# Kernel tuning notes

Hardware: AMD Instinct MI355X
Metric: run time of the kernel (lower is better)

The kernel has to match this reference:

```python
import jax, jax.numpy as jnp
import numpy as np

B, T, D = 4, 2048, 1024
N_HEADS = 16
D_HEAD = D // N_HEADS


def setup_inputs() -> dict:
    key = jax.random.key(0)
    ks = jax.random.split(key, 5)
    s = 1.0 / np.sqrt(D)
    return {
        "x": jax.random.normal(ks[0], (B, T, D), dtype=jnp.float32),
        "wq": jax.random.normal(ks[1], (D, D), dtype=jnp.float32) * s,
        "wk": jax.random.normal(ks[2], (D, D), dtype=jnp.float32) * s,
        "wv": jax.random.normal(ks[3], (D, D), dtype=jnp.float32) * s,
        "wo": jax.random.normal(ks[4], (D, D), dtype=jnp.float32) * s,
    }


def reference(x, wq, wk, wv, wo):
    # nn.Linear applies y = x @ W^T (no bias)
    b, t, c = x.shape
    def heads(w):
        return (x @ w.T).reshape(b, t, N_HEADS, D_HEAD).transpose(0, 2, 1, 3)  # (B,H,T,d)
    q, k, v = heads(wq), heads(wk), heads(wv)
    scale = 1.0 / np.sqrt(D_HEAD).astype(np.float32)
    att = jnp.einsum('bhqd,bhkd->bhqk', q, k) * scale
    causal = jnp.tril(jnp.ones((t, t), dtype=bool))
    att = jnp.where(causal[None, None], att, -jnp.inf)
    att = jax.nn.softmax(att, axis=-1)
    # dropout is identity in eval / p acts as 0 for the deterministic reference
    y = jnp.einsum('bhqk,bhkd->bhqd', att, v)
    y = y.transpose(0, 2, 1, 3).reshape(b, t, c)
    return y @ wo.T
```

## Files before the change

### kernel.cpp

```cpp
#include <hip/hip_runtime.h>

#define B_ 4
#define T_ 2048
#define D_ 1024
#define H_ 16
#define DH_ 64
#define M_ (B_*T_)
#define KP 72

typedef __attribute__((ext_vector_type(8))) short short8;
typedef __attribute__((ext_vector_type(4))) float f32x4;
typedef __attribute__((ext_vector_type(4))) unsigned short u16x4;
typedef _Float16 half4f __attribute__((ext_vector_type(4)));

__device__ __forceinline__ unsigned short f2bf(float f) {
  unsigned int u = __float_as_uint(f);
  u += 0x7FFFu + ((u >> 16) & 1u);
  return (unsigned short)(u >> 16);
}

__device__ __forceinline__ void async_copy16(const void* g, void* l) {
  __builtin_amdgcn_global_load_lds(
      (const __attribute__((address_space(1))) unsigned int*)(g),
      (__attribute__((address_space(3))) unsigned int*)(l),
      16, 0, 0);
}

__device__ __forceinline__ f32x4 mfma32(short8 a, short8 b, f32x4 c) {
  return __builtin_amdgcn_mfma_f32_16x16x32_bf16(a, b, c, 0, 0, 0);
}

__global__ __launch_bounds__(256) void cvt_f32_to_bf16(
    const float* __restrict__ in, unsigned short* __restrict__ out, int n4) {
  int i = blockIdx.x * 256 + threadIdx.x;
  if (i >= n4) return;
  const float4 v = reinterpret_cast<const float4*>(in)[i];
  u16x4 o;
  o.x = f2bf(v.x); o.y = f2bf(v.y); o.z = f2bf(v.z); o.w = f2bf(v.w);
  reinterpret_cast<u16x4*>(out)[i] = o;
}

__global__ __launch_bounds__(256) void gemm_qkv(
    const unsigned short* __restrict__ A,
    const unsigned short* __restrict__ Wq,
    const unsigned short* __restrict__ Wk,
    const unsigned short* __restrict__ Wv,
    unsigned short* __restrict__ Qo,
    unsigned short* __restrict__ Ko,
    _Float16* __restrict__ Vo) {
  __shared__ __align__(16) unsigned short ldsA[128*32];
  __shared__ __align__(16) unsigned short ldsB[128*32];
  const int tid = threadIdx.x;
  const int w = tid >> 6, lane = tid & 63;
  const int quad = lane >> 4, l16 = lane & 15;
  const int wr = (w >> 1) * 64, wc = (w & 1) * 64;
  const int m0 = blockIdx.x * 128;
  const int seg = blockIdx.y >> 3;
  const int n0 = (blockIdx.y & 7) * 128;
  const unsigned short* Bt = (seg == 0) ? Wq : ((seg == 1) ? Wk : Wv);

  const unsigned short* gA = A  + (size_t)(m0 + w*32 + (lane >> 2)) * D_ + (lane & 3) * 8;
  const unsigned short* gB = Bt + (size_t)(n0 + w*32 + (lane >> 2)) * D_ + (lane & 3) * 8;
  unsigned short* lA = ldsA + (w*32)*32;
  unsigned short* lB = ldsB + (w*32)*32;

  f32x4 acc[4][4] = {};

  for (int k0 = 0; k0 < D_; k0 += 32) {
    __syncthreads();
#pragma unroll
    for (int g = 0; g < 2; ++g) {
      async_copy16(gA + (size_t)k0 + (size_t)g*16*D_, lA + g*16*32);
      async_copy16(gB + (size_t)k0 + (size_t)g*16*D_, lB + g*16*32);
    }
    __syncthreads();
    short8 af[4], bfr[4];
#pragma unroll
    for (int t = 0; t < 4; ++t) {
      af[t]  = *reinterpret_cast<const short8*>(ldsA + (wr + t*16 + l16)*32 + quad*8);
      bfr[t] = *reinterpret_cast<const short8*>(ldsB + (wc + t*16 + l16)*32 + quad*8);
    }
#pragma unroll
    for (int i = 0; i < 4; ++i)
#pragma unroll
      for (int j = 0; j < 4; ++j)
        acc[i][j] = mfma32(af[i], bfr[j], acc[i][j]);
  }

#pragma unroll
  for (int i = 0; i < 4; ++i) {
#pragma unroll
    for (int j = 0; j < 4; ++j) {
      if (seg == 2) {
        const int colc = n0 + wc + j*16 + l16;
        const int hh = colc >> 6, dd = colc & (DH_ - 1);
        const int row0 = m0 + wr + i*16 + quad*4;
        const int bb = row0 >> 11, t0 = row0 & (T_ - 1);
        half4f vh = {(_Float16)acc[i][j][0], (_Float16)acc[i][j][1],
                     (_Float16)acc[i][j][2], (_Float16)acc[i][j][3]};
        *reinterpret_cast<half4f*>(
            &Vo[(size_t)((bb*H_ + hh)*DH_ + dd)*T_ + t0]) = vh;
      } else {
        unsigned short* out = (seg == 0) ? Qo : Ko;
        const float scl = (seg == 0) ? (0.125f * 1.44269504089f) : 1.f;
#pragma unroll
        for (int r = 0; r < 4; ++r) {
          const int row = m0 + wr + i*16 + quad*4 + r;
          const int col = n0 + wc + j*16 + l16;
          out[(size_t)row * D_ + col] = f2bf(acc[i][j][r] * scl);
        }
      }
    }
  }
}

__global__ __launch_bounds__(256) void gemm_out(
    const unsigned short* __restrict__ A,
    const unsigned short* __restrict__ Bt,
    float* __restrict__ Cout) {
  __shared__ __align__(16) unsigned short ldsA[128*32];
  __shared__ __align__(16) unsigned short ldsB[128*32];
  const int tid = threadIdx.x;
  const int w = tid >> 6, lane = tid & 63;
  const int quad = lane >> 4, l16 = lane & 15;
  const int wr = (w >> 1) * 64, wc = (w & 1) * 64;
  const int m0 = blockIdx.x * 128, n0 = blockIdx.y * 128;

  const unsigned short* gA = A  + (size_t)(m0 + w*32 + (lane >> 2)) * D_ + (lane & 3) * 8;
  const unsigned short* gB = Bt + (size_t)(n0 + w*32 + (lane >> 2)) * D_ + (lane & 3) * 8;
  unsigned short* lA = ldsA + (w*32)*32;
  unsigned short* lB = ldsB + (w*32)*32;

  f32x4 acc[4][4] = {};
  for (int k0 = 0; k0 < D_; k0 += 32) {
    __syncthreads();
#pragma unroll
    for (int g = 0; g < 2; ++g) {
      async_copy16(gA + (size_t)k0 + (size_t)g*16*D_, lA + g*16*32);
      async_copy16(gB + (size_t)k0 + (size_t)g*16*D_, lB + g*16*32);
    }
    __syncthreads();
    short8 af[4], bfr[4];
#pragma unroll
    for (int t = 0; t < 4; ++t) {
      af[t]  = *reinterpret_cast<const short8*>(ldsA + (wr + t*16 + l16)*32 + quad*8);
      bfr[t] = *reinterpret_cast<const short8*>(ldsB + (wc + t*16 + l16)*32 + quad*8);
    }
#pragma unroll
    for (int i = 0; i < 4; ++i)
#pragma unroll
      for (int j = 0; j < 4; ++j)
        acc[i][j] = mfma32(af[i], bfr[j], acc[i][j]);
  }
#pragma unroll
  for (int i = 0; i < 4; ++i)
#pragma unroll
    for (int j = 0; j < 4; ++j)
#pragma unroll
      for (int r = 0; r < 4; ++r)
        Cout[(size_t)(m0 + wr + i*16 + quad*4 + r) * D_ + n0 + wc + j*16 + l16] =
            acc[i][j][r];
}

__global__ __launch_bounds__(256) void flash_attn(
    const unsigned short* __restrict__ Q,
    const unsigned short* __restrict__ K,
    const _Float16* __restrict__ Vt,
    unsigned short* __restrict__ Y) {
  __shared__ __align__(16) unsigned short Kl[2][64*KP];
  __shared__ __align__(16) _Float16      Vl[2][64*KP];
  const int px = blockIdx.x, h = blockIdx.y, b = blockIdx.z;
  const int tid = threadIdx.x;
  const int w = tid >> 6, lane = tid & 63, quad = lane >> 4, l16 = lane & 15;
  const int hc = h * DH_;
  const size_t bh = (size_t)(b*H_ + h);

  const int sr = tid >> 2, sc = tid & 3;
  const unsigned short* Kg0 = K + ((size_t)(b*T_) + sr) * D_ + hc + sc*16;
  const _Float16*       Vg0 = Vt + (bh*DH_ + sr) * T_ + sc*16;

  uint4 kr0, kr1, vr0, vr1;
  auto loadKV = [&](int kt) {
    const unsigned short* kg = Kg0 + (size_t)kt * 64 * D_;
    const _Float16*       vg = Vg0 + kt * 64;
    kr0 = *reinterpret_cast<const uint4*>(kg);
    kr1 = *reinterpret_cast<const uint4*>(kg + 8);
    vr0 = *reinterpret_cast<const uint4*>(vg);
    vr1 = *reinterpret_cast<const uint4*>(vg + 8);
  };
  auto writeKV = [&](int bi) {
    *reinterpret_cast<uint4*>(&Kl[bi][sr*KP + sc*16])     = kr0;
    *reinterpret_cast<uint4*>(&Kl[bi][sr*KP + sc*16 + 8]) = kr1;
    *reinterpret_cast<uint4*>(&Vl[bi][sr*KP + sc*16])     = vr0;
    *reinterpret_cast<uint4*>(&Vl[bi][sr*KP + sc*16 + 8]) = vr1;
  };

#pragma unroll
  for (int pi = 0; pi < 2; ++pi) {
    const int it = pi ? (31 - px) : px;
    const int qg0 = it*64 + w*16;

    short8 bq[2];
#pragma unroll
    for (int ks = 0; ks < 2; ++ks)
      bq[ks] = *reinterpret_cast<const short8*>(
          Q + (size_t)(b*T_ + qg0 + l16) * D_ + hc + ks*32 + quad*8);

    f32x4 o[4] = {};
    float rs = 0.f;
    const int ktmax = it;

    __syncthreads();
    loadKV(0);
    writeKV(0);
    __syncthreads();

    for (int kt = 0; kt <= ktmax; ++kt) {
      const int cur = kt & 1;
      if (kt < ktmax) loadKV(kt + 1);
      const bool diag = (kt == ktmax);
      const int smax = diag ? w : 3;
      const int diagS = diag ? w : -1;
      for (int s = 0; s <= smax; ++s) {
        const short8 ka0 = *reinterpret_cast<const short8*>(
            &Kl[cur][(s*16 + l16)*KP + quad*8]);
        const short8 ka1 = *reinterpret_cast<const short8*>(
            &Kl[cur][(s*16 + l16)*KP + 32 + quad*8]);
        f32x4 z = {0.f, 0.f, 0.f, 0.f};
        z = mfma32(ka0, bq[0], z);
        z = mfma32(ka1, bq[1], z);
        float p[4];
        const bool dsub = (s == diagS);
#pragma unroll
        for (int r = 0; r < 4; ++r) {
          float pv = __builtin_amdgcn_exp2f(z[r]);
          if (dsub && (quad*4 + r > l16)) pv = 0.f;
          p[r] = pv;
          rs += pv;
        }
        const half4f pf = {(_Float16)p[0], (_Float16)p[1],
                           (_Float16)p[2], (_Float16)p[3]};
#pragma unroll
        for (int dt = 0; dt < 4; ++dt) {
          const half4f vf = *reinterpret_cast<const half4f*>(
              &Vl[cur][(dt*16 + l16)*KP + s*16 + quad*4]);
          o[dt] = __builtin_amdgcn_mfma_f32_16x16x16f16(vf, pf, o[dt], 0, 0, 0);
        }
      }
      if (kt < ktmax) {
        __syncthreads();
        writeKV(cur ^ 1);
        __syncthreads();
      }
    }

    float rt = rs;
    rt += __shfl_xor(rt, 16);
    rt += __shfl_xor(rt, 32);
    const float inv = 1.f / rt;

#pragma unroll
    for (int dt = 0; dt < 4; ++dt) {
      u16x4 yo;
      yo.x = f2bf(o[dt][0] * inv);
      yo.y = f2bf(o[dt][1] * inv);
      yo.z = f2bf(o[dt][2] * inv);
      yo.w = f2bf(o[dt][3] * inv);
      *reinterpret_cast<u16x4*>(
          &Y[(size_t)(b*T_ + qg0 + l16) * D_ + hc + dt*16 + quad*4]) = yo;
    }
  }
}

extern "C" void kernel_launch(void* const* d_in, const int* in_sizes, int n_in,
                              void* d_out, int out_size, void* d_ws, size_t ws_size,
                              hipStream_t stream) {
  const float* x  = (const float*)d_in[0];
  const float* wq = (const float*)d_in[1];
  const float* wk = (const float*)d_in[2];
  const float* wv = (const float*)d_in[3];
  const float* wo = (const float*)d_in[4];

  unsigned short* xb  = (unsigned short*)d_ws;
  unsigned short* wqb = xb  + (size_t)M_ * D_;
  unsigned short* wkb = wqb + (size_t)D_ * D_;
  unsigned short* wvb = wkb + (size_t)D_ * D_;
  unsigned short* wob = wvb + (size_t)D_ * D_;
  unsigned short* q   = wob + (size_t)D_ * D_;
  unsigned short* k   = q   + (size_t)M_ * D_;
  _Float16*       vt  = (_Float16*)(k + (size_t)M_ * D_);
  unsigned short* y   = (unsigned short*)(vt + (size_t)M_ * D_);

  const int nx4 = M_ * D_ / 4, nw4 = D_ * D_ / 4;
  cvt_f32_to_bf16<<<nx4 / 256, 256, 0, stream>>>(x,  xb,  nx4);
  cvt_f32_to_bf16<<<nw4 / 256, 256, 0, stream>>>(wq, wqb, nw4);
  cvt_f32_to_bf16<<<nw4 / 256, 256, 0, stream>>>(wk, wkb, nw4);
  cvt_f32_to_bf16<<<nw4 / 256, 256, 0, stream>>>(wv, wvb, nw4);
  cvt_f32_to_bf16<<<nw4 / 256, 256, 0, stream>>>(wo, wob, nw4);

  gemm_qkv<<<dim3(M_ / 128, 24), 256, 0, stream>>>(xb, wqb, wkb, wvb, q, k, vt);

  flash_attn<<<dim3(16, H_, B_), 256, 0, stream>>>(q, k, vt, y);

  gemm_out<<<dim3(M_ / 128, D_ / 128), 256, 0, stream>>>(y, wob, (float*)d_out);
}
```

Baseline: 277.4 us.

## Give each attention wave two query tiles and fuse the five conversion kernels

The flash attention block drops to two waves of 128 threads, and each wave now handles 32 query rows as two 16-row tiles. Every K/V fragment read from LDS is therefore reused for twice as many MFMAs. The softmax row sum is now computed by an MFMA against a ones vector instead of scalar adds and shuffles, and the grid order changes so batch-head varies fastest. The five fp32-to-bf16 conversion launches are merged into one kernel to cut launch overhead. Trade-offs are higher register pressure, fewer waves per block to hide latency, and some wasted diagonal work.

```diff
diff --git a/kernel.cpp b/kernel.cpp
--- a/kernel.cpp
+++ b/kernel.cpp
@@ -29,15 +29,29 @@
 __device__ __forceinline__ f32x4 mfma32(short8 a, short8 b, f32x4 c) {
   return __builtin_amdgcn_mfma_f32_16x16x32_bf16(a, b, c, 0, 0, 0);
 }
-
-__global__ __launch_bounds__(256) void cvt_f32_to_bf16(
-    const float* __restrict__ in, unsigned short* __restrict__ out, int n4) {
+__device__ __forceinline__ f32x4 mfma16h(half4f a, half4f b, f32x4 c) {
+  return __builtin_amdgcn_mfma_f32_16x16x16f16(a, b, c, 0, 0, 0);
+}
+
+#define NX4 (M_*D_/4)
+#define NW4 (D_*D_/4)
+__global__ __launch_bounds__(256) void cvt_all(
+    const float* __restrict__ x,  const float* __restrict__ wq,
+    const float* __restrict__ wk, const float* __restrict__ wv,
+    const float* __restrict__ wo, unsigned short* __restrict__ xb,
+    unsigned short* __restrict__ wqb, unsigned short* __restrict__ wkb,
+    unsigned short* __restrict__ wvb, unsigned short* __restrict__ wob) {
   int i = blockIdx.x * 256 + threadIdx.x;
-  if (i >= n4) return;
-  const float4 v = reinterpret_cast<const float4*>(in)[i];
+  const float* src; unsigned short* dst; int off;
+  if (i < NX4)             { src = x;  dst = xb;  off = i; }
+  else if (i < NX4 + NW4)  { src = wq; dst = wqb; off = i - NX4; }
+  else if (i < NX4 + 2*NW4){ src = wk; dst = wkb; off = i - NX4 - NW4; }
+  else if (i < NX4 + 3*NW4){ src = wv; dst = wvb; off = i - NX4 - 2*NW4; }
+  else                     { src = wo; dst = wob; off = i - NX4 - 3*NW4; }
+  const float4 v = reinterpret_cast<const float4*>(src)[off];
   u16x4 o;
   o.x = f2bf(v.x); o.y = f2bf(v.y); o.z = f2bf(v.z); o.w = f2bf(v.w);
-  reinterpret_cast<u16x4*>(out)[i] = o;
+  reinterpret_cast<u16x4*>(dst)[off] = o;
 }
 
 __global__ __launch_bounds__(256) void gemm_qkv(
@@ -162,52 +176,58 @@
             acc[i][j][r];
 }
 
-__global__ __launch_bounds__(256) void flash_attn(
+__global__ __launch_bounds__(128) void flash_attn(
     const unsigned short* __restrict__ Q,
     const unsigned short* __restrict__ K,
     const _Float16* __restrict__ Vt,
     unsigned short* __restrict__ Y) {
   __shared__ __align__(16) unsigned short Kl[2][64*KP];
   __shared__ __align__(16) _Float16      Vl[2][64*KP];
-  const int px = blockIdx.x, h = blockIdx.y, b = blockIdx.z;
+  const int bh = blockIdx.x, px = blockIdx.y;
+  const int h = bh & (H_ - 1), b = bh >> 4;
   const int tid = threadIdx.x;
   const int w = tid >> 6, lane = tid & 63, quad = lane >> 4, l16 = lane & 15;
   const int hc = h * DH_;
-  const size_t bh = (size_t)(b*H_ + h);
-
-  const int sr = tid >> 2, sc = tid & 3;
-  const unsigned short* Kg0 = K + ((size_t)(b*T_) + sr) * D_ + hc + sc*16;
-  const _Float16*       Vg0 = Vt + (bh*DH_ + sr) * T_ + sc*16;
-
-  uint4 kr0, kr1, vr0, vr1;
+
+  const int sr = tid >> 1, sco = (tid & 1) * 32;
+  const unsigned short* Kg0 = K + ((size_t)(b*T_) + sr) * D_ + hc + sco;
+  const _Float16*       Vg0 = Vt + ((size_t)bh * DH_ + sr) * T_ + sco;
+
+  uint4 kr[4], vr[4];
   auto loadKV = [&](int kt) {
     const unsigned short* kg = Kg0 + (size_t)kt * 64 * D_;
     const _Float16*       vg = Vg0 + kt * 64;
-    kr0 = *reinterpret_cast<const uint4*>(kg);
-    kr1 = *reinterpret_cast<const uint4*>(kg + 8);
-    vr0 = *reinterpret_cast<const uint4*>(vg);
-    vr1 = *reinterpret_cast<const uint4*>(vg + 8);
+#pragma unroll
+    for (int j = 0; j < 4; ++j) {
+      kr[j] = *reinterpret_cast<const uint4*>(kg + j*8);
+      vr[j] = *reinterpret_cast<const uint4*>(vg + j*8);
+    }
   };
   auto writeKV = [&](int bi) {
-    *reinterpret_cast<uint4*>(&Kl[bi][sr*KP + sc*16])     = kr0;
-    *reinterpret_cast<uint4*>(&Kl[bi][sr*KP + sc*16 + 8]) = kr1;
-    *reinterpret_cast<uint4*>(&Vl[bi][sr*KP + sc*16])     = vr0;
-    *reinterpret_cast<uint4*>(&Vl[bi][sr*KP + sc*16 + 8]) = vr1;
+#pragma unroll
+    for (int j = 0; j < 4; ++j) {
+      *reinterpret_cast<uint4*>(&Kl[bi][sr*KP + sco + j*8]) = kr[j];
+      *reinterpret_cast<uint4*>(&Vl[bi][sr*KP + sco + j*8]) = vr[j];
+    }
   };
+
+  const half4f vones = {(_Float16)1.f, (_Float16)1.f, (_Float16)1.f, (_Float16)1.f};
 
 #pragma unroll
   for (int pi = 0; pi < 2; ++pi) {
     const int it = pi ? (31 - px) : px;
-    const int qg0 = it*64 + w*16;
-
-    short8 bq[2];
-#pragma unroll
-    for (int ks = 0; ks < 2; ++ks)
-      bq[ks] = *reinterpret_cast<const short8*>(
-          Q + (size_t)(b*T_ + qg0 + l16) * D_ + hc + ks*32 + quad*8);
-
-    f32x4 o[4] = {};
-    float rs = 0.f;
+    const int qg0 = it*64 + w*32;
+
+    short8 bq[2][2];
+#pragma unroll
+    for (int qt = 0; qt < 2; ++qt)
+#pragma unroll
+      for (int ks = 0; ks < 2; ++ks)
+        bq[qt][ks] = *reinterpret_cast<const short8*>(
+            Q + (size_t)(b*T_ + qg0 + qt*16 + l16) * D_ + hc + ks*32 + quad*8);
+
+    f32x4 o[2][4] = {};
+    f32x4 osum[2] = {};
     const int ktmax = it;
 
     __syncthreads();
@@ -219,32 +239,40 @@
       const int cur = kt & 1;
       if (kt < ktmax) loadKV(kt + 1);
       const bool diag = (kt == ktmax);
-      const int smax = diag ? w : 3;
-      const int diagS = diag ? w : -1;
+      const int smax = diag ? (2*w + 1) : 3;
       for (int s = 0; s <= smax; ++s) {
         const short8 ka0 = *reinterpret_cast<const short8*>(
             &Kl[cur][(s*16 + l16)*KP + quad*8]);
         const short8 ka1 = *reinterpret_cast<const short8*>(
             &Kl[cur][(s*16 + l16)*KP + 32 + quad*8]);
-        f32x4 z = {0.f, 0.f, 0.f, 0.f};
-        z = mfma32(ka0, bq[0], z);
-        z = mfma32(ka1, bq[1], z);
-        float p[4];
-        const bool dsub = (s == diagS);
-#pragma unroll
-        for (int r = 0; r < 4; ++r) {
-          float pv = __builtin_amdgcn_exp2f(z[r]);
-          if (dsub && (quad*4 + r > l16)) pv = 0.f;
-          p[r] = pv;
-          rs += pv;
+        const bool skip0 = diag && (s == 2*w + 1);
+        const bool m0d   = diag && (s == 2*w);
+        const bool m1d   = diag && (s == 2*w + 1);
+        half4f pf[2];
+#pragma unroll
+        for (int qt = 0; qt < 2; ++qt) {
+          if (qt == 0 && skip0) continue;
+          f32x4 z = {0.f, 0.f, 0.f, 0.f};
+          z = mfma32(ka0, bq[qt][0], z);
+          z = mfma32(ka1, bq[qt][1], z);
+          const bool dm = qt ? m1d : m0d;
+          float p[4];
+#pragma unroll
+          for (int r = 0; r < 4; ++r) {
+            float pv = __builtin_amdgcn_exp2f(z[r]);
+            if (dm && (quad*4 + r > l16)) pv = 0.f;
+            p[r] = pv;
+          }
+          pf[qt] = half4f{(_Float16)p[0], (_Float16)p[1],
+                          (_Float16)p[2], (_Float16)p[3]};
+          osum[qt] = mfma16h(vones, pf[qt], osum[qt]);
         }
-        const half4f pf = {(_Float16)p[0], (_Float16)p[1],
-                           (_Float16)p[2], (_Float16)p[3]};
 #pragma unroll
         for (int dt = 0; dt < 4; ++dt) {
           const half4f vf = *reinterpret_cast<const half4f*>(
               &Vl[cur][(dt*16 + l16)*KP + s*16 + quad*4]);
-          o[dt] = __builtin_amdgcn_mfma_f32_16x16x16f16(vf, pf, o[dt], 0, 0, 0);
+          if (!skip0) o[0][dt] = mfma16h(vf, pf[0], o[0][dt]);
+          o[1][dt] = mfma16h(vf, pf[1], o[1][dt]);
         }
       }
       if (kt < ktmax) {
@@ -254,20 +282,19 @@
       }
     }
 
-    float rt = rs;
-    rt += __shfl_xor(rt, 16);
-    rt += __shfl_xor(rt, 32);
-    const float inv = 1.f / rt;
-
-#pragma unroll
-    for (int dt = 0; dt < 4; ++dt) {
-      u16x4 yo;
-      yo.x = f2bf(o[dt][0] * inv);
-      yo.y = f2bf(o[dt][1] * inv);
-      yo.z = f2bf(o[dt][2] * inv);
-      yo.w = f2bf(o[dt][3] * inv);
-      *reinterpret_cast<u16x4*>(
-          &Y[(size_t)(b*T_ + qg0 + l16) * D_ + hc + dt*16 + quad*4]) = yo;
+#pragma unroll
+    for (int qt = 0; qt < 2; ++qt) {
+      const float inv = 1.f / osum[qt][0];
+#pragma unroll
+      for (int dt = 0; dt < 4; ++dt) {
+        u16x4 yo;
+        yo.x = f2bf(o[qt][dt][0] * inv);
+        yo.y = f2bf(o[qt][dt][1] * inv);
+        yo.z = f2bf(o[qt][dt][2] * inv);
+        yo.w = f2bf(o[qt][dt][3] * inv);
+        *reinterpret_cast<u16x4*>(
+            &Y[(size_t)(b*T_ + qg0 + qt*16 + l16) * D_ + hc + dt*16 + quad*4]) = yo;
+      }
     }
   }
 }
@@ -291,16 +318,12 @@
   _Float16*       vt  = (_Float16*)(k + (size_t)M_ * D_);
   unsigned short* y   = (unsigned short*)(vt + (size_t)M_ * D_);
 
-  const int nx4 = M_ * D_ / 4, nw4 = D_ * D_ / 4;
-  cvt_f32_to_bf16<<<nx4 / 256, 256, 0, stream>>>(x,  xb,  nx4);
-  cvt_f32_to_bf16<<<nw4 / 256, 256, 0, stream>>>(wq, wqb, nw4);
-  cvt_f32_to_bf16<<<nw4 / 256, 256, 0, stream>>>(wk, wkb, nw4);
-  cvt_f32_to_bf16<<<nw4 / 256, 256, 0, stream>>>(wv, wvb, nw4);
-  cvt_f32_to_bf16<<<nw4 / 256, 256, 0, stream>>>(wo, wob, nw4);
+  const int ncv = (NX4 + 4*NW4 + 255) / 256;
+  cvt_all<<<ncv, 256, 0, stream>>>(x, wq, wk, wv, wo, xb, wqb, wkb, wvb, wob);
 
   gemm_qkv<<<dim3(M_ / 128, 24), 256, 0, stream>>>(xb, wqb, wkb, wvb, q, k, vt);
 
-  flash_attn<<<dim3(16, H_, B_), 256, 0, stream>>>(q, k, vt, y);
+  flash_attn<<<dim3(64, 16), 128, 0, stream>>>(q, k, vt, y);
 
   gemm_out<<<dim3(M_ / 128, D_ / 128), 256, 0, stream>>>(y, wob, (float*)d_out);
 }
```

After: 356.2 us. 1.28x slower.
